# Performance work log

Measured on AMD Instinct MI355X. Metric: run time of the kernel, lower is better.

## Reference

```python
import jax, jax.numpy as jnp
import numpy as np

N = 100000      # num nodes
E = 3200000     # num edges
R = 8           # num relations
C_IN, HID, C_OUT = 128, 64, 64


def rgcn_conv(x, W, root, bias, src, dst, etype):
    """One RGCNConv layer (PyG semantics, mean aggregation per relation).
    out[i] = bias + x[i] @ root + sum_r mean_{j in N_r(i)} x[j] @ W[r]
    """
    n = x.shape[0]
    # transform-then-gather: [R, N, H] avoids per-edge [E, C, H] matmuls
    xW = jnp.einsum('nc,rch->rnh', x, W)
    msg = xW[etype, src]                              # [E, H]
    # per-(relation, target-node) in-degree for mean normalization
    seg = etype * n + dst
    deg = jax.ops.segment_sum(jnp.ones((src.shape[0],), dtype=x.dtype), seg,
                              num_segments=R * n)      # [R*N]
    msg = msg / jnp.maximum(deg[seg], 1.0)[:, None]
    agg = jax.ops.segment_sum(msg, dst, num_segments=n)  # [N, H]
    return agg + x @ root + bias


def setup_inputs() -> dict:
    key = jax.random.key(0)
    ks = jax.random.split(key, 9)
    x = jax.random.normal(ks[0], (N, C_IN), dtype=jnp.float32)
    edge_index = jax.random.randint(ks[1], (2, E), 0, N)
    edge_type = jax.random.randint(ks[2], (E,), 0, R)
    s1 = 1.0 / np.sqrt(C_IN)
    s2 = 1.0 / np.sqrt(HID)
    W1 = jax.random.normal(ks[3], (R, C_IN, HID), dtype=jnp.float32) * s1
    root1 = jax.random.normal(ks[4], (C_IN, HID), dtype=jnp.float32) * s1
    b1 = jnp.zeros((HID,), dtype=jnp.float32)
    W2 = jax.random.normal(ks[5], (R, HID, C_OUT), dtype=jnp.float32) * s2
    root2 = jax.random.normal(ks[6], (HID, C_OUT), dtype=jnp.float32) * s2
    b2 = jnp.zeros((C_OUT,), dtype=jnp.float32)
    return {"x": x, "edge_index": edge_index, "edge_type": edge_type,
            "W1": W1, "root1": root1, "b1": b1,
            "W2": W2, "root2": root2, "b2": b2}


def reference(x, edge_index, edge_type, W1, root1, b1, W2, root2, b2):
    src, dst = edge_index[0], edge_index[1]
    h = rgcn_conv(x, W1, root1, b1, src, dst, edge_type)
    h = jax.nn.relu(h)  # dropout p=0.0 is identity
    out = rgcn_conv(h, W2, root2, b2, src, dst, edge_type)
    return out
```

## Files before the change

kernel.cpp:

```cpp
#include <hip/hip_runtime.h>

#define N_NODES 100000
#define N_EDGES 3200000
#define R_REL   8
#define C_IN    128
#define HID     64
#define WCOLS   576

#define NBUCK 500
#define NPB   200
#define NBLK  256
#define CHUNK 12500
#define NCELL (NBUCK * NBLK)
#define BCAP  7424
#define PREPC 432

typedef __attribute__((ext_vector_type(8))) short  short8;
typedef __attribute__((ext_vector_type(4))) float  float4v;

__device__ __forceinline__ float bf2f(unsigned short u) {
    union { unsigned int i; float f; } v; v.i = ((unsigned int)u) << 16; return v.f;
}
__device__ __forceinline__ unsigned short f2bf(float f) {
    union { float f; unsigned int i; } v; v.f = f;
    unsigned int r = v.i + 0x7FFFu + ((v.i >> 16) & 1u);
    return (unsigned short)(r >> 16);
}
__device__ __forceinline__ float rl_f(float v, int j) {
    union { float f; int i; } a, b; a.f = v;
    b.i = __builtin_amdgcn_readlane(a.i, j);
    return b.f;
}

__device__ __forceinline__ int block_exscan_1024(int v, int tid, int* wsum, int* tot) {
    __syncthreads();
    const int lane = tid & 63, wid = tid >> 6;
    int s = v;
#pragma unroll
    for (int d = 1; d < 64; d <<= 1) {
        int t = __shfl_up(s, d, 64);
        if (lane >= d) s += t;
    }
    if (lane == 63) wsum[wid] = s;
    __syncthreads();
    if (wid == 0) {
        int ws = (lane < 16) ? wsum[lane] : 0;
#pragma unroll
        for (int d = 1; d < 16; d <<= 1) {
            int t = __shfl_up(ws, d, 64);
            if (lane >= d) ws += t;
        }
        if (lane < 16) wsum[lane] = ws;
    }
    __syncthreads();
    int wexcl = (wid == 0) ? 0 : wsum[wid - 1];
    if (tot) *tot = wsum[15];
    return wexcl + s - v;
}

__global__ __launch_bounds__(1024)
void edge_sort_local(const int* __restrict__ src, const int* __restrict__ dst,
                     const int* __restrict__ et,
                     const float* __restrict__ W1, const float* __restrict__ root1,
                     const float* __restrict__ W2, const float* __restrict__ root2,
                     unsigned short* __restrict__ BT1, unsigned short* __restrict__ BT2,
                     unsigned int* __restrict__ esort,
                     int* __restrict__ bcountT, int* __restrict__ lstartT) {
    __shared__ int cnt[NBUCK], cur[NBUCK], wsum[16];
    __shared__ unsigned int sedge[CHUNK];
    const int blk = blockIdx.x, tid = threadIdx.x;
    const int e0 = blk * CHUNK;

    if (tid < PREPC) {
        int idx = blk * PREPC + tid;
        const int T1 = WCOLS * C_IN;
        if (idx < T1) {
            int c = idx / C_IN, k = idx % C_IN;
            float v;
            if (c < 512) { int r = c >> 6, h = c & 63; v = W1[r * (C_IN * 64) + k * 64 + h]; }
            else         { v = root1[k * 64 + (c - 512)]; }
            BT1[idx] = f2bf(v);
        } else {
            int j = idx - T1;
            int c = j / HID, k = j % HID;
            float v;
            if (c < 512) { int r = c >> 6, h = c & 63; v = W2[r * (HID * 64) + k * 64 + h]; }
            else         { v = root2[k * 64 + (c - 512)]; }
            BT2[j] = f2bf(v);
        }
    }

    for (int i = tid; i < NBUCK; i += 1024) cnt[i] = 0;
    __syncthreads();
    for (int i = tid; i < CHUNK; i += 1024)
        atomicAdd(&cnt[dst[e0 + i] / NPB], 1);
    __syncthreads();

    int v = (tid < NBUCK) ? cnt[tid] : 0;
    int ex = block_exscan_1024(v, tid, wsum, nullptr);
    if (tid < NBUCK) {
        cur[tid] = ex;
        bcountT[blk * NBUCK + tid] = v;
        lstartT[blk * NBUCK + tid] = ex;
    }
    __syncthreads();

    for (int i = tid; i < CHUNK; i += 1024) {
        int d = dst[e0 + i];
        int b = d / NPB;
        int pos = atomicAdd(&cur[b], 1);
        sedge[pos] = ((unsigned int)src[e0 + i] << 11) |
                     ((unsigned int)(d - b * NPB) << 3) | (unsigned int)et[e0 + i];
    }
    __syncthreads();
    for (int i = tid; i < CHUNK; i += 1024) esort[e0 + i] = sedge[i];
}

__global__ __launch_bounds__(1024)
void bucket_build(const unsigned int* __restrict__ esort,
                  const int* __restrict__ bcountT, const int* __restrict__ lstartT,
                  unsigned int* __restrict__ elist,
                  int* __restrict__ rowstart8) {
    __shared__ int   cnt[2048], cur[2048];
    __shared__ int   rlen_s[NBLK], rpos[NBLK], rloff[NBLK], wsum[16];
    __shared__ unsigned int sedge[BCAP];
    __shared__ unsigned int selist[BCAP];

    const int b = blockIdx.x, tid = threadIdx.x;

    for (int i = tid; i < 2048; i += 1024) cnt[i] = 0;
    int myrl = 0, myls = 0;
    if (tid < NBLK) {
        myrl = bcountT[tid * NBUCK + b];
        myls = lstartT[tid * NBUCK + b];
        rlen_s[tid] = myrl;
        rpos[tid] = tid * CHUNK + myls;
    }

    int total;
    int rex = block_exscan_1024(myrl, tid, wsum, &total);
    if (tid < NBLK) rloff[tid] = rex;

    int seg0;
    (void)block_exscan_1024(myls, tid, wsum, &seg0);
    __syncthreads();
    const bool fits = (total <= BCAP);

    {
        const int run = tid >> 2, sub = tid & 3;
        const int len = rlen_s[run], lp = rpos[run], ro = rloff[run];
        for (int k = sub; k < len; k += 4) {
            unsigned int e = esort[lp + k];
            if (fits) sedge[ro + k] = e;
            atomicAdd(&cnt[(int)((e >> 3) & 255u) * 8 + (int)(e & 7u)], 1);
        }
    }
    __syncthreads();

    int base = tid * 2;
    int c0 = cnt[base], c1 = cnt[base + 1];
    int ex2 = block_exscan_1024(c0 + c1, tid, wsum, nullptr);
    cur[base] = ex2; cur[base + 1] = ex2 + c0;
    __syncthreads();

    for (int i = tid; i < NPB * 8; i += 1024)
        rowstart8[(b * NPB) * 8 + i] = seg0 + cur[i];
    if (b == NBUCK - 1 && tid == 0) rowstart8[N_NODES * 8] = N_EDGES;
    __syncthreads();

    if (fits) {
        for (int i = tid; i < total; i += 1024) {
            unsigned int e = sedge[i];
            int r = (int)(e & 7u);
            int j = (int)((e >> 3) & 255u) * 8 + r;
            int p = atomicAdd(&cur[j], 1);
            selist[p] = (e >> 11) * WCOLS + (unsigned int)(r * 64);
        }
        __syncthreads();
        for (int i = tid; i < total; i += 1024)
            elist[seg0 + i] = selist[i];
    } else {
        const int run = tid >> 2, sub = tid & 3;
        const int len = rlen_s[run], lp = rpos[run];
        for (int k = sub; k < len; k += 4) {
            unsigned int e = esort[lp + k];
            int r = (int)(e & 7u);
            int j = (int)((e >> 3) & 255u) * 8 + r;
            int p = atomicAdd(&cur[j], 1);
            elist[seg0 + p] = (e >> 11) * WCOLS + (unsigned int)(r * 64);
        }
    }
}

__global__ __launch_bounds__(512)
void gemm_l1(const float* __restrict__ A,
             const unsigned short* __restrict__ BT,
             unsigned short* __restrict__ Out, int nrows) {
    constexpr int K = C_IN;
    constexpr int LDB = K + 8;
    __shared__ __align__(16) unsigned short Blds[2][64 * LDB];
    __shared__ __align__(16) unsigned short stage[8][16 * 64];

    const int wave = threadIdx.x >> 6, lane = threadIdx.x & 63;
    const int l15 = lane & 15, quad = lane >> 4;
    const int rowbase = blockIdx.x * 128 + wave * 16;
    int arow = rowbase + l15;
    if (arow >= nrows) arow = nrows - 1;

    short8 afrag[4];
#pragma unroll
    for (int ks = 0; ks < 4; ++ks) {
        const float* p = A + (size_t)arow * K + ks * 32 + quad * 8;
        float4v u0 = *(const float4v*)p;
        float4v u1 = *(const float4v*)(p + 4);
        short8 f;
        f[0] = (short)f2bf(u0[0]); f[1] = (short)f2bf(u0[1]);
        f[2] = (short)f2bf(u0[2]); f[3] = (short)f2bf(u0[3]);
        f[4] = (short)f2bf(u1[0]); f[5] = (short)f2bf(u1[1]);
        f[6] = (short)f2bf(u1[2]); f[7] = (short)f2bf(u1[3]);
        afrag[ks] = f;
    }

    for (int i = threadIdx.x; i < 1024; i += 512) {
        int r = i >> 4, c = (i & 15) * 8;
        *(uint4*)&Blds[0][r * LDB + c] = *(const uint4*)(BT + r * K + c);
    }
    __syncthreads();

    int cur = 0;
    for (int chunk = 0; chunk < 9; ++chunk) {
        uint4 p0, p1;
        const int i0 = threadIdx.x, i1 = threadIdx.x + 512;
        if (chunk < 8) {
            const unsigned short* src = BT + (size_t)(chunk + 1) * 64 * K;
            p0 = *(const uint4*)(src + (i0 >> 4) * K + (i0 & 15) * 8);
            p1 = *(const uint4*)(src + (i1 >> 4) * K + (i1 & 15) * 8);
        }

        float4v acc[4];
#pragma unroll
        for (int ct = 0; ct < 4; ++ct) { acc[ct][0] = 0.f; acc[ct][1] = 0.f; acc[ct][2] = 0.f; acc[ct][3] = 0.f; }
#pragma unroll
        for (int ct = 0; ct < 4; ++ct)
#pragma unroll
            for (int ks = 0; ks < 4; ++ks) {
                short8 bfrag = *(const short8*)(&Blds[cur][(ct * 16 + l15) * LDB + ks * 32 + quad * 8]);
                acc[ct] = __builtin_amdgcn_mfma_f32_16x16x32_bf16(afrag[ks], bfrag, acc[ct], 0, 0, 0);
            }

#pragma unroll
        for (int ct = 0; ct < 4; ++ct)
#pragma unroll
            for (int r = 0; r < 4; ++r)
                stage[wave][(quad * 4 + r) * 64 + ct * 16 + l15] = f2bf(acc[ct][r]);
        {
            int r = lane >> 2, j = lane & 3;
            int orow = rowbase + r;
            if (orow < nrows) {
#pragma unroll
                for (int p = 0; p < 2; ++p) {
                    int c0 = (j + p * 4) * 8;
                    uint4 v = *(const uint4*)&stage[wave][r * 64 + c0];
                    *(uint4*)(Out + (size_t)orow * WCOLS + chunk * 64 + c0) = v;
                }
            }
        }

        if (chunk < 8) {
            *(uint4*)&Blds[cur ^ 1][(i0 >> 4) * LDB + (i0 & 15) * 8] = p0;
            *(uint4*)&Blds[cur ^ 1][(i1 >> 4) * LDB + (i1 & 15) * 8] = p1;
            cur ^= 1;
        }
        __syncthreads();
    }
}

__global__ __launch_bounds__(512)
void gemm_l2(const unsigned short* __restrict__ A,
             const unsigned short* __restrict__ BT,
             unsigned short* __restrict__ Out, int nrows) {
    constexpr int K = HID;
    constexpr int LDB = K + 8;
    __shared__ __align__(16) unsigned short Blds[WCOLS * LDB];
    __shared__ __align__(16) unsigned short stage[8][16 * 64];

    const int wave = threadIdx.x >> 6, lane = threadIdx.x & 63;
    const int l15 = lane & 15, quad = lane >> 4;

    for (int i = threadIdx.x; i < WCOLS * K / 8; i += 512) {
        int c = i >> 3, kv = (i & 7) * 8;
        *(uint4*)&Blds[c * LDB + kv] = *(const uint4*)(BT + c * K + kv);
    }
    __syncthreads();

    const int ntiles = (nrows + 127) / 128;
    for (int t = blockIdx.x; t < ntiles; t += gridDim.x) {
        const int rowbase = t * 128 + wave * 16;
        int arow = rowbase + l15;
        if (arow >= nrows) arow = nrows - 1;
        short8 afrag[2];
#pragma unroll
        for (int ks = 0; ks < 2; ++ks)
            afrag[ks] = *(const short8*)(A + (size_t)arow * K + ks * 32 + quad * 8);

        for (int chunk = 0; chunk < 9; ++chunk) {
            float4v acc[4];
#pragma unroll
            for (int ct = 0; ct < 4; ++ct) { acc[ct][0] = 0.f; acc[ct][1] = 0.f; acc[ct][2] = 0.f; acc[ct][3] = 0.f; }
#pragma unroll
            for (int ct = 0; ct < 4; ++ct)
#pragma unroll
                for (int ks = 0; ks < 2; ++ks) {
                    short8 bfrag = *(const short8*)(&Blds[(chunk * 64 + ct * 16 + l15) * LDB + ks * 32 + quad * 8]);
                    acc[ct] = __builtin_amdgcn_mfma_f32_16x16x32_bf16(afrag[ks], bfrag, acc[ct], 0, 0, 0);
                }

#pragma unroll
            for (int ct = 0; ct < 4; ++ct)
#pragma unroll
                for (int r = 0; r < 4; ++r)
                    stage[wave][(quad * 4 + r) * 64 + ct * 16 + l15] = f2bf(acc[ct][r]);
            {
                int r = lane >> 2, j = lane & 3;
                int orow = rowbase + r;
                if (orow < nrows) {
#pragma unroll
                    for (int p = 0; p < 2; ++p) {
                        int c0 = (j + p * 4) * 8;
                        uint4 v = *(const uint4*)&stage[wave][r * 64 + c0];
                        *(uint4*)(Out + (size_t)orow * WCOLS + chunk * 64 + c0) = v;
                    }
                }
            }
        }
    }
}

template <int MODE>
__global__ __launch_bounds__(256)
void agg_fused(const unsigned short* __restrict__ XW,
               const unsigned int* __restrict__ elist,
               const int* __restrict__ rowstart8,
               const float* __restrict__ bias,
               void* __restrict__ outp) {
    const int wave = threadIdx.x >> 6, lane = threadIdx.x & 63;
    const int n = blockIdx.x * 4 + wave;
    int r9 = 0;
    if (lane < 9) r9 = rowstart8[n * 8 + lane];
    const int b0 = __builtin_amdgcn_readlane(r9, 0);
    const int b1 = __builtin_amdgcn_readlane(r9, 1);
    const int b2 = __builtin_amdgcn_readlane(r9, 2);
    const int b3 = __builtin_amdgcn_readlane(r9, 3);
    const int b4 = __builtin_amdgcn_readlane(r9, 4);
    const int b5 = __builtin_amdgcn_readlane(r9, 5);
    const int b6 = __builtin_amdgcn_readlane(r9, 6);
    const int b7 = __builtin_amdgcn_readlane(r9, 7);
    const int b8 = __builtin_amdgcn_readlane(r9, 8);
    const int beg = b0, end = b8;

    auto invlen = [](int a, int bnd) {
        int l = bnd - a; return 1.0f / (float)(l > 1 ? l : 1);
    };
    const float il0 = invlen(b0, b1), il1 = invlen(b1, b2);
    const float il2 = invlen(b2, b3), il3 = invlen(b3, b4);
    const float il4 = invlen(b4, b5), il5 = invlen(b5, b6);
    const float il6 = invlen(b6, b7), il7 = invlen(b7, b8);

    const unsigned short* XWl = XW + lane;

    float acc = 0.f;
    int i = beg;
    while (i < end) {
        int m = end - i; if (m > 64) m = 64;
        int idx = i + lane; if (idx >= end) idx = end - 1;
        unsigned int ub = elist[idx];
        float wb = il0;
        wb = (idx >= b1) ? il1 : wb;
        wb = (idx >= b2) ? il2 : wb;
        wb = (idx >= b3) ? il3 : wb;
        wb = (idx >= b4) ? il4 : wb;
        wb = (idx >= b5) ? il5 : wb;
        wb = (idx >= b6) ? il6 : wb;
        wb = (idx >= b7) ? il7 : wb;

        int j = 0;
        for (; j + 16 <= m; j += 16) {
            float vv[16], ww[16];
#pragma unroll
            for (int t = 0; t < 16; ++t) {
                unsigned int u = (unsigned int)__builtin_amdgcn_readlane((int)ub, j + t);
                ww[t] = rl_f(wb, j + t);
                vv[t] = bf2f(XWl[u]);
            }
#pragma unroll
            for (int t = 0; t < 16; ++t) acc += ww[t] * vv[t];
        }
        for (; j + 4 <= m; j += 4) {
            float vv[4], ww[4];
#pragma unroll
            for (int t = 0; t < 4; ++t) {
                unsigned int u = (unsigned int)__builtin_amdgcn_readlane((int)ub, j + t);
                ww[t] = rl_f(wb, j + t);
                vv[t] = bf2f(XWl[u]);
            }
#pragma unroll
            for (int t = 0; t < 4; ++t) acc += ww[t] * vv[t];
        }
        for (; j < m; ++j) {
            unsigned int u = (unsigned int)__builtin_amdgcn_readlane((int)ub, j);
            float w = rl_f(wb, j);
            acc += w * bf2f(XWl[u]);
        }
        i += m;
    }

    float res = acc + bf2f(XW[(size_t)n * WCOLS + 512 + lane]) + bias[lane];
    if (MODE == 0) {
        res = res > 0.f ? res : 0.f;
        ((unsigned short*)outp)[(size_t)n * 64 + lane] = f2bf(res);
    } else {
        ((float*)outp)[(size_t)n * 64 + lane] = res;
    }
}

extern "C" void kernel_launch(void* const* d_in, const int* in_sizes, int n_in,
                              void* d_out, int out_size, void* d_ws, size_t ws_size,
                              hipStream_t stream) {
    const float* x     = (const float*)d_in[0];
    const int*   eidx  = (const int*)d_in[1];
    const int*   etyp  = (const int*)d_in[2];
    const float* W1    = (const float*)d_in[3];
    const float* root1 = (const float*)d_in[4];
    const float* b1    = (const float*)d_in[5];
    const float* W2    = (const float*)d_in[6];
    const float* root2 = (const float*)d_in[7];
    const float* b2    = (const float*)d_in[8];
    float*       out   = (float*)d_out;

    char* ws = (char*)d_ws;
    size_t off = 0;
    auto alloc = [&](size_t bytes) { char* p = ws + off; off += (bytes + 255) & ~(size_t)255; return p; };

    unsigned short* xW       = (unsigned short*)alloc((size_t)N_NODES * WCOLS * 2);
    unsigned short* h        = (unsigned short*)alloc((size_t)N_NODES * HID * 2);
    unsigned int*   elist    = (unsigned int*)alloc((size_t)N_EDGES * 4);
    int*            rowstart8= (int*)alloc(((size_t)N_NODES * 8 + 1) * 4);
    unsigned short* BT1      = (unsigned short*)alloc((size_t)WCOLS * C_IN * 2);
    unsigned short* BT2      = (unsigned short*)alloc((size_t)WCOLS * HID * 2);

    unsigned int* esort   = (unsigned int*)xW;
    int*          bcountT = (int*)((char*)xW + (size_t)N_EDGES * 4);
    int*          lstartT = bcountT + NCELL;

    const int* srcp = eidx;
    const int* dstp = eidx + N_EDGES;

    edge_sort_local<<<NBLK, 1024, 0, stream>>>(srcp, dstp, etyp,
                                               W1, root1, W2, root2, BT1, BT2,
                                               esort, bcountT, lstartT);
    bucket_build<<<NBUCK, 1024, 0, stream>>>(esort, bcountT, lstartT, elist, rowstart8);

    const int gemm1_grid = (N_NODES + 127) / 128;
    const int agg_grid   = N_NODES / 4;

    gemm_l1<<<gemm1_grid, 512, 0, stream>>>(x, BT1, xW, N_NODES);
    agg_fused<0><<<agg_grid, 256, 0, stream>>>(xW, elist, rowstart8, b1, (void*)h);

    gemm_l2<<<256, 512, 0, stream>>>(h, BT2, xW, N_NODES);
    agg_fused<1><<<agg_grid, 256, 0, stream>>>(xW, elist, rowstart8, b2, (void*)out);
}
```

Baseline: 367.0 us.

## Fuse edge local sort with layer-1 GEMM in one heterogeneous launch

```diff
diff --git a/kernel.cpp b/kernel.cpp
--- a/kernel.cpp
+++ b/kernel.cpp
@@ -13,7 +13,7 @@
 #define CHUNK 12500
 #define NCELL (NBUCK * NBLK)
 #define BCAP  7424
-#define PREPC 432
+#define GEMM1_BLKS 391
 
 typedef __attribute__((ext_vector_type(8))) short  short8;
 typedef __attribute__((ext_vector_type(4))) float  float4v;
@@ -58,48 +58,58 @@
     return wexcl + s - v;
 }
 
-__global__ __launch_bounds__(1024)
-void edge_sort_local(const int* __restrict__ src, const int* __restrict__ dst,
-                     const int* __restrict__ et,
-                     const float* __restrict__ W1, const float* __restrict__ root1,
-                     const float* __restrict__ W2, const float* __restrict__ root2,
-                     unsigned short* __restrict__ BT1, unsigned short* __restrict__ BT2,
-                     unsigned int* __restrict__ esort,
-                     int* __restrict__ bcountT, int* __restrict__ lstartT) {
-    __shared__ int cnt[NBUCK], cur[NBUCK], wsum[16];
-    __shared__ unsigned int sedge[CHUNK];
-    const int blk = blockIdx.x, tid = threadIdx.x;
+__global__ void prep_wcat(const float* __restrict__ W1,
+                          const float* __restrict__ root1,
+                          const float* __restrict__ W2,
+                          const float* __restrict__ root2,
+                          unsigned short* __restrict__ BT1,
+                          unsigned short* __restrict__ BT2) {
+    int idx = blockIdx.x * 256 + threadIdx.x;
+    const int T1 = WCOLS * C_IN;
+    const int T2 = WCOLS * HID;
+    if (idx < T1) {
+        int c = idx / C_IN, k = idx % C_IN;
+        float v;
+        if (c < 512) { int r = c >> 6, h = c & 63; v = W1[r * (C_IN * 64) + k * 64 + h]; }
+        else         { v = root1[k * 64 + (c - 512)]; }
+        BT1[idx] = f2bf(v);
+    } else if (idx < T1 + T2) {
+        int j = idx - T1;
+        int c = j / HID, k = j % HID;
+        float v;
+        if (c < 512) { int r = c >> 6, h = c & 63; v = W2[r * (HID * 64) + k * 64 + h]; }
+        else         { v = root2[k * 64 + (c - 512)]; }
+        BT2[j] = f2bf(v);
+    }
+}
+
+struct SortMem {
+    int cnt[NBUCK], cur[NBUCK], wsum[16];
+    unsigned int sedge[CHUNK];
+};
+struct GemmMem {
+    unsigned short Blds[2][64 * 136];
+    unsigned short stage[16][1024];
+};
+
+__device__ __forceinline__ void sort_body(char* smem, int blk,
+        const int* __restrict__ src, const int* __restrict__ dst,
+        const int* __restrict__ et, unsigned int* __restrict__ esort,
+        int* __restrict__ bcountT, int* __restrict__ lstartT) {
+    SortMem* sm = (SortMem*)smem;
+    const int tid = threadIdx.x;
     const int e0 = blk * CHUNK;
 
-    if (tid < PREPC) {
-        int idx = blk * PREPC + tid;
-        const int T1 = WCOLS * C_IN;
-        if (idx < T1) {
-            int c = idx / C_IN, k = idx % C_IN;
-            float v;
-            if (c < 512) { int r = c >> 6, h = c & 63; v = W1[r * (C_IN * 64) + k * 64 + h]; }
-            else         { v = root1[k * 64 + (c - 512)]; }
-            BT1[idx] = f2bf(v);
-        } else {
-            int j = idx - T1;
-            int c = j / HID, k = j % HID;
-            float v;
-            if (c < 512) { int r = c >> 6, h = c & 63; v = W2[r * (HID * 64) + k * 64 + h]; }
-            else         { v = root2[k * 64 + (c - 512)]; }
-            BT2[j] = f2bf(v);
-        }
-    }
-
-    for (int i = tid; i < NBUCK; i += 1024) cnt[i] = 0;
+    for (int i = tid; i < NBUCK; i += 1024) sm->cnt[i] = 0;
     __syncthreads();
     for (int i = tid; i < CHUNK; i += 1024)
-        atomicAdd(&cnt[dst[e0 + i] / NPB], 1);
-    __syncthreads();
-
-    int v = (tid < NBUCK) ? cnt[tid] : 0;
-    int ex = block_exscan_1024(v, tid, wsum, nullptr);
+        atomicAdd(&sm->cnt[dst[e0 + i] / NPB], 1);
+    __syncthreads();
+
+    int v = (tid < NBUCK) ? sm->cnt[tid] : 0;
+    int ex = block_exscan_1024(v, tid, sm->wsum, nullptr);
     if (tid < NBUCK) {
-        cur[tid] = ex;
+        sm->cur[tid] = ex;
         bcountT[blk * NBUCK + tid] = v;
         lstartT[blk * NBUCK + tid] = ex;
     }
@@ -108,12 +118,106 @@
     for (int i = tid; i < CHUNK; i += 1024) {
         int d = dst[e0 + i];
         int b = d / NPB;
-        int pos = atomicAdd(&cur[b], 1);
-        sedge[pos] = ((unsigned int)src[e0 + i] << 11) |
-                     ((unsigned int)(d - b * NPB) << 3) | (unsigned int)et[e0 + i];
-    }
-    __syncthreads();
-    for (int i = tid; i < CHUNK; i += 1024) esort[e0 + i] = sedge[i];
+        int pos = atomicAdd(&sm->cur[b], 1);
+        sm->sedge[pos] = ((unsigned int)src[e0 + i] << 11) |
+                         ((unsigned int)(d - b * NPB) << 3) | (unsigned int)et[e0 + i];
+    }
+    __syncthreads();
+    for (int i = tid; i < CHUNK; i += 1024) esort[e0 + i] = sm->sedge[i];
+}
+
+__device__ __forceinline__ void gemm1_body(char* smem, int gblk,
+        const float* __restrict__ A, const unsigned short* __restrict__ BT,
+        unsigned short* __restrict__ Out, int nrows) {
+    GemmMem* gm = (GemmMem*)smem;
+    const int tid = threadIdx.x;
+    const int wave = tid >> 6, lane = tid & 63;
+    const int l15 = lane & 15, quad = lane >> 4;
+    const int rowbase = gblk * 256 + wave * 16;
+    int arow = rowbase + l15;
+    if (arow >= nrows) arow = nrows - 1;
+
+    short8 afrag[4];
+#pragma unroll
+    for (int ks = 0; ks < 4; ++ks) {
+        const float* p = A + (size_t)arow * C_IN + ks * 32 + quad * 8;
+        float4v u0 = *(const float4v*)p;
+        float4v u1 = *(const float4v*)(p + 4);
+        short8 f;
+        f[0] = (short)f2bf(u0[0]); f[1] = (short)f2bf(u0[1]);
+        f[2] = (short)f2bf(u0[2]); f[3] = (short)f2bf(u0[3]);
+        f[4] = (short)f2bf(u1[0]); f[5] = (short)f2bf(u1[1]);
+        f[6] = (short)f2bf(u1[2]); f[7] = (short)f2bf(u1[3]);
+        afrag[ks] = f;
+    }
+
+    {
+        int r = tid >> 4, c = (tid & 15) * 8;
+        *(uint4*)&gm->Blds[0][r * 136 + c] = *(const uint4*)(BT + r * C_IN + c);
+    }
+    __syncthreads();
+
+    int cur = 0;
+    for (int chunk = 0; chunk < 9; ++chunk) {
+        uint4 p0;
+        if (chunk < 8) {
+            const unsigned short* src = BT + (size_t)(chunk + 1) * 64 * C_IN;
+            p0 = *(const uint4*)(src + (tid >> 4) * C_IN + (tid & 15) * 8);
+        }
+
+        float4v acc[4];
+#pragma unroll
+        for (int ct = 0; ct < 4; ++ct) { acc[ct][0] = 0.f; acc[ct][1] = 0.f; acc[ct][2] = 0.f; acc[ct][3] = 0.f; }
+#pragma unroll
+        for (int ct = 0; ct < 4; ++ct)
+#pragma unroll
+            for (int ks = 0; ks < 4; ++ks) {
+                short8 bfrag = *(const short8*)(&gm->Blds[cur][(ct * 16 + l15) * 136 + ks * 32 + quad * 8]);
+                acc[ct] = __builtin_amdgcn_mfma_f32_16x16x32_bf16(afrag[ks], bfrag, acc[ct], 0, 0, 0);
+            }
+
+#pragma unroll
+        for (int ct = 0; ct < 4; ++ct)
+#pragma unroll
+            for (int r = 0; r < 4; ++r)
+                gm->stage[wave][(quad * 4 + r) * 64 + ct * 16 + l15] = f2bf(acc[ct][r]);
+        {
+            int r = lane >> 2, j = lane & 3;
+            int orow = rowbase + r;
+            if (orow < nrows) {
+#pragma unroll
+                for (int p = 0; p < 2; ++p) {
+                    int c0 = (j + p * 4) * 8;
+                    uint4 v = *(const uint4*)&gm->stage[wave][r * 64 + c0];
+                    *(uint4*)(Out + (size_t)orow * WCOLS + chunk * 64 + c0) = v;
+                }
+            }
+        }
+
+        if (chunk < 8) {
+            *(uint4*)&gm->Blds[cur ^ 1][(tid >> 4) * 136 + (tid & 15) * 8] = p0;
+            cur ^= 1;
+        }
+        __syncthreads();
+    }
+}
+
+__global__ __launch_bounds__(1024)
+void sort_gemm1(const int* __restrict__ src, const int* __restrict__ dst,
+                const int* __restrict__ et,
+                unsigned int* __restrict__ esort,
+                int* __restrict__ bcountT, int* __restrict__ lstartT,
+                const float* __restrict__ x, const unsigned short* __restrict__ BT1,
+                unsigned short* __restrict__ xW) {
+    __shared__ __align__(16) char smem[sizeof(GemmMem) > sizeof(SortMem) ?
+                                       sizeof(GemmMem) : sizeof(SortMem)];
+    const int bx = blockIdx.x;
+    if (bx < 2 * NBLK) {
+        if (!(bx & 1)) sort_body(smem, bx >> 1, src, dst, et, esort, bcountT, lstartT);
+        else           gemm1_body(smem, bx >> 1, x, BT1, xW, N_NODES);
+    } else {
+        gemm1_body(smem, NBLK + (bx - 2 * NBLK), x, BT1, xW, N_NODES);
+    }
 }
 
 __global__ __launch_bounds__(1024)
@@ -189,89 +293,6 @@
             int p = atomicAdd(&cur[j], 1);
             elist[seg0 + p] = (e >> 11) * WCOLS + (unsigned int)(r * 64);
         }
-    }
-}
-
-__global__ __launch_bounds__(512)
-void gemm_l1(const float* __restrict__ A,
-             const unsigned short* __restrict__ BT,
-             unsigned short* __restrict__ Out, int nrows) {
-    constexpr int K = C_IN;
-    constexpr int LDB = K + 8;
-    __shared__ __align__(16) unsigned short Blds[2][64 * LDB];
-    __shared__ __align__(16) unsigned short stage[8][16 * 64];
-
-    const int wave = threadIdx.x >> 6, lane = threadIdx.x & 63;
-    const int l15 = lane & 15, quad = lane >> 4;
-    const int rowbase = blockIdx.x * 128 + wave * 16;
-    int arow = rowbase + l15;
-    if (arow >= nrows) arow = nrows - 1;
-
-    short8 afrag[4];
-#pragma unroll
-    for (int ks = 0; ks < 4; ++ks) {
-        const float* p = A + (size_t)arow * K + ks * 32 + quad * 8;
-        float4v u0 = *(const float4v*)p;
-        float4v u1 = *(const float4v*)(p + 4);
-        short8 f;
-        f[0] = (short)f2bf(u0[0]); f[1] = (short)f2bf(u0[1]);
-        f[2] = (short)f2bf(u0[2]); f[3] = (short)f2bf(u0[3]);
-        f[4] = (short)f2bf(u1[0]); f[5] = (short)f2bf(u1[1]);
-        f[6] = (short)f2bf(u1[2]); f[7] = (short)f2bf(u1[3]);
-        afrag[ks] = f;
-    }
-
-    for (int i = threadIdx.x; i < 1024; i += 512) {
-        int r = i >> 4, c = (i & 15) * 8;
-        *(uint4*)&Blds[0][r * LDB + c] = *(const uint4*)(BT + r * K + c);
-    }
-    __syncthreads();
-
-    int cur = 0;
-    for (int chunk = 0; chunk < 9; ++chunk) {
-        uint4 p0, p1;
-        const int i0 = threadIdx.x, i1 = threadIdx.x + 512;
-        if (chunk < 8) {
-            const unsigned short* src = BT + (size_t)(chunk + 1) * 64 * K;
-            p0 = *(const uint4*)(src + (i0 >> 4) * K + (i0 & 15) * 8);
-            p1 = *(const uint4*)(src + (i1 >> 4) * K + (i1 & 15) * 8);
-        }
-
-        float4v acc[4];
-#pragma unroll
-        for (int ct = 0; ct < 4; ++ct) { acc[ct][0] = 0.f; acc[ct][1] = 0.f; acc[ct][2] = 0.f; acc[ct][3] = 0.f; }
-#pragma unroll
-        for (int ct = 0; ct < 4; ++ct)
-#pragma unroll
-            for (int ks = 0; ks < 4; ++ks) {
-                short8 bfrag = *(const short8*)(&Blds[cur][(ct * 16 + l15) * LDB + ks * 32 + quad * 8]);
-                acc[ct] = __builtin_amdgcn_mfma_f32_16x16x32_bf16(afrag[ks], bfrag, acc[ct], 0, 0, 0);
-            }
-
-#pragma unroll
-        for (int ct = 0; ct < 4; ++ct)
-#pragma unroll
-            for (int r = 0; r < 4; ++r)
-                stage[wave][(quad * 4 + r) * 64 + ct * 16 + l15] = f2bf(acc[ct][r]);
-        {
-            int r = lane >> 2, j = lane & 3;
-            int orow = rowbase + r;
-            if (orow < nrows) {
-#pragma unroll
-                for (int p = 0; p < 2; ++p) {
-                    int c0 = (j + p * 4) * 8;
-                    uint4 v = *(const uint4*)&stage[wave][r * 64 + c0];
-                    *(uint4*)(Out + (size_t)orow * WCOLS + chunk * 64 + c0) = v;
-                }
-            }
-        }
-
-        if (chunk < 8) {
-            *(uint4*)&Blds[cur ^ 1][(i0 >> 4) * LDB + (i0 & 15) * 8] = p0;
-            *(uint4*)&Blds[cur ^ 1][(i1 >> 4) * LDB + (i1 & 15) * 8] = p1;
-            cur ^= 1;
-        }
-        __syncthreads();
     }
 }
 
@@ -447,23 +468,23 @@
     int*            rowstart8= (int*)alloc(((size_t)N_NODES * 8 + 1) * 4);
     unsigned short* BT1      = (unsigned short*)alloc((size_t)WCOLS * C_IN * 2);
     unsigned short* BT2      = (unsigned short*)alloc((size_t)WCOLS * HID * 2);
-
-    unsigned int* esort   = (unsigned int*)xW;
-    int*          bcountT = (int*)((char*)xW + (size_t)N_EDGES * 4);
-    int*          lstartT = bcountT + NCELL;
+    int*            bcountT  = (int*)alloc((size_t)NCELL * 4);
+    int*            lstartT  = (int*)alloc((size_t)NCELL * 4);
+
+    unsigned int* esort = (unsigned int*)h;
 
     const int* srcp = eidx;
     const int* dstp = eidx + N_EDGES;
 
-    edge_sort_local<<<NBLK, 1024, 0, stream>>>(srcp, dstp, etyp,
-                                               W1, root1, W2, root2, BT1, BT2,
-                                               esort, bcountT, lstartT);
+    prep_wcat<<<(WCOLS * (C_IN + HID) + 255) / 256, 256, 0, stream>>>(W1, root1, W2, root2, BT1, BT2);
+
+    sort_gemm1<<<2 * NBLK + (GEMM1_BLKS - NBLK), 1024, 0, stream>>>(
+        srcp, dstp, etyp, esort, bcountT, lstartT, x, BT1, xW);
+
     bucket_build<<<NBUCK, 1024, 0, stream>>>(esort, bcountT, lstartT, elist, rowstart8);
 
-    const int gemm1_grid = (N_NODES + 127) / 128;
-    const int agg_grid   = N_NODES / 4;
-
-    gemm_l1<<<gemm1_grid, 512, 0, stream>>>(x, BT1, xW, N_NODES);
+    const int agg_grid = N_NODES / 4;
+
     agg_fused<0><<<agg_grid, 256, 0, stream>>>(xW, elist, rowstart8, b1, (void*)h);
 
     gemm_l2<<<256, 512, 0, stream>>>(h, BT2, xW, N_NODES);
```

New measurement: 373.7 us. About the same (+1.8%).

## Double-buffer B chunks in layer-2 GEMM and launch one block per tile

Applied to the files above, without the earlier changes.

```diff
diff --git a/kernel.cpp b/kernel.cpp
--- a/kernel.cpp
+++ b/kernel.cpp
@@ -281,58 +281,68 @@
              unsigned short* __restrict__ Out, int nrows) {
     constexpr int K = HID;
     constexpr int LDB = K + 8;
-    __shared__ __align__(16) unsigned short Blds[WCOLS * LDB];
+    __shared__ __align__(16) unsigned short Blds[2][64 * LDB];
     __shared__ __align__(16) unsigned short stage[8][16 * 64];
 
     const int wave = threadIdx.x >> 6, lane = threadIdx.x & 63;
     const int l15 = lane & 15, quad = lane >> 4;
-
-    for (int i = threadIdx.x; i < WCOLS * K / 8; i += 512) {
-        int c = i >> 3, kv = (i & 7) * 8;
-        *(uint4*)&Blds[c * LDB + kv] = *(const uint4*)(BT + c * K + kv);
-    }
-    __syncthreads();
-
-    const int ntiles = (nrows + 127) / 128;
-    for (int t = blockIdx.x; t < ntiles; t += gridDim.x) {
-        const int rowbase = t * 128 + wave * 16;
-        int arow = rowbase + l15;
-        if (arow >= nrows) arow = nrows - 1;
-        short8 afrag[2];
-#pragma unroll
-        for (int ks = 0; ks < 2; ++ks)
-            afrag[ks] = *(const short8*)(A + (size_t)arow * K + ks * 32 + quad * 8);
-
-        for (int chunk = 0; chunk < 9; ++chunk) {
-            float4v acc[4];
-#pragma unroll
-            for (int ct = 0; ct < 4; ++ct) { acc[ct][0] = 0.f; acc[ct][1] = 0.f; acc[ct][2] = 0.f; acc[ct][3] = 0.f; }
-#pragma unroll
-            for (int ct = 0; ct < 4; ++ct)
-#pragma unroll
-                for (int ks = 0; ks < 2; ++ks) {
-                    short8 bfrag = *(const short8*)(&Blds[(chunk * 64 + ct * 16 + l15) * LDB + ks * 32 + quad * 8]);
-                    acc[ct] = __builtin_amdgcn_mfma_f32_16x16x32_bf16(afrag[ks], bfrag, acc[ct], 0, 0, 0);
+    const int rowbase = blockIdx.x * 128 + wave * 16;
+    int arow = rowbase + l15;
+    if (arow >= nrows) arow = nrows - 1;
+
+    short8 afrag[2];
+#pragma unroll
+    for (int ks = 0; ks < 2; ++ks)
+        afrag[ks] = *(const short8*)(A + (size_t)arow * K + ks * 32 + quad * 8);
+
+    {
+        int r = threadIdx.x >> 3, c = (threadIdx.x & 7) * 8;
+        *(uint4*)&Blds[0][r * LDB + c] = *(const uint4*)(BT + r * K + c);
+    }
+    __syncthreads();
+
+    int cur = 0;
+    for (int chunk = 0; chunk < 9; ++chunk) {
+        uint4 p0;
+        if (chunk < 8) {
+            const unsigned short* src = BT + (size_t)(chunk + 1) * 64 * K;
+            p0 = *(const uint4*)(src + (threadIdx.x >> 3) * K + (threadIdx.x & 7) * 8);
+        }
+
+        float4v acc[4];
+#pragma unroll
+        for (int ct = 0; ct < 4; ++ct) { acc[ct][0] = 0.f; acc[ct][1] = 0.f; acc[ct][2] = 0.f; acc[ct][3] = 0.f; }
+#pragma unroll
+        for (int ct = 0; ct < 4; ++ct)
+#pragma unroll
+            for (int ks = 0; ks < 2; ++ks) {
+                short8 bfrag = *(const short8*)(&Blds[cur][(ct * 16 + l15) * LDB + ks * 32 + quad * 8]);
+                acc[ct] = __builtin_amdgcn_mfma_f32_16x16x32_bf16(afrag[ks], bfrag, acc[ct], 0, 0, 0);
+            }
+
+#pragma unroll
+        for (int ct = 0; ct < 4; ++ct)
+#pragma unroll
+            for (int r = 0; r < 4; ++r)
+                stage[wave][(quad * 4 + r) * 64 + ct * 16 + l15] = f2bf(acc[ct][r]);
+        {
+            int r = lane >> 2, j = lane & 3;
+            int orow = rowbase + r;
+            if (orow < nrows) {
+#pragma unroll
+                for (int p = 0; p < 2; ++p) {
+                    int c0 = (j + p * 4) * 8;
+                    uint4 v = *(const uint4*)&stage[wave][r * 64 + c0];
+                    *(uint4*)(Out + (size_t)orow * WCOLS + chunk * 64 + c0) = v;
                 }
-
-#pragma unroll
-            for (int ct = 0; ct < 4; ++ct)
-#pragma unroll
-                for (int r = 0; r < 4; ++r)
-                    stage[wave][(quad * 4 + r) * 64 + ct * 16 + l15] = f2bf(acc[ct][r]);
-            {
-                int r = lane >> 2, j = lane & 3;
-                int orow = rowbase + r;
-                if (orow < nrows) {
-#pragma unroll
-                    for (int p = 0; p < 2; ++p) {
-                        int c0 = (j + p * 4) * 8;
-                        uint4 v = *(const uint4*)&stage[wave][r * 64 + c0];
-                        *(uint4*)(Out + (size_t)orow * WCOLS + chunk * 64 + c0) = v;
-                    }
-                }
-            }
-        }
+            }
+        }
+
+        if (chunk < 8) {
+            *(uint4*)&Blds[cur ^ 1][(threadIdx.x >> 3) * LDB + (threadIdx.x & 7) * 8] = p0;
+            cur ^= 1;
+        }
+        __syncthreads();
     }
 }
 
@@ -460,12 +470,12 @@
                                                esort, bcountT, lstartT);
     bucket_build<<<NBUCK, 1024, 0, stream>>>(esort, bcountT, lstartT, elist, rowstart8);
 
-    const int gemm1_grid = (N_NODES + 127) / 128;
-    const int agg_grid   = N_NODES / 4;
-
-    gemm_l1<<<gemm1_grid, 512, 0, stream>>>(x, BT1, xW, N_NODES);
+    const int gemm_grid = (N_NODES + 127) / 128;
+    const int agg_grid  = N_NODES / 4;
+
+    gemm_l1<<<gemm_grid, 512, 0, stream>>>(x, BT1, xW, N_NODES);
     agg_fused<0><<<agg_grid, 256, 0, stream>>>(xW, elist, rowstart8, b1, (void*)h);
 
-    gemm_l2<<<256, 512, 0, stream>>>(h, BT2, xW, N_NODES);
+    gemm_l2<<<gemm_grid, 512, 0, stream>>>(h, BT2, xW, N_NODES);
     agg_fused<1><<<agg_grid, 256, 0, stream>>>(xW, elist, rowstart8, b2, (void*)out);
 }
```

New measurement: 363.4 us. No clear change (-1.0%).
